# Kernel optimization log

Hardware: AMD Instinct MI355X
Metric: run time of the kernel (lower is better)

Reference implementation:

```python
import jax, jax.numpy as jnp
import numpy as np

N_FACTORS = 4
N_ITERATIONS = 2
N_LAYERS = 2
N_USERS = 50000
N_ITEMS = 50000
EMB_DIM = 128
N_EDGES = 2_000_000
EPS = 1e-12


def setup_inputs() -> dict:
    key = jax.random.key(0)
    k1, k2, k3, k4 = jax.random.split(key, 4)
    n_nodes = N_USERS + N_ITEMS
    return {
        "user_emb": jax.random.normal(k1, (N_USERS, EMB_DIM), dtype=jnp.float32) * 0.1,
        "item_emb": jax.random.normal(k2, (N_ITEMS, EMB_DIM), dtype=jnp.float32) * 0.1,
        "all_h_list": jax.random.randint(k3, (N_EDGES,), 0, n_nodes, dtype=jnp.int32),
        "all_t_list": jax.random.randint(k4, (N_EDGES,), 0, n_nodes, dtype=jnp.int32),
    }


def _l2norm(x):
    # F.normalize(x, dim=1): x / max(||x||_2, eps)
    n = jnp.sqrt(jnp.sum(x * x, axis=1, keepdims=True))
    return x / jnp.maximum(n, EPS)


def _star_routing(user_emb, item_emb, h, t):
    n_nodes = user_emb.shape[0] + item_emb.shape[0]
    E = h.shape[0]
    ego = jnp.concatenate([user_emb, item_emb], axis=0)          # [N, D]
    A_values = jnp.ones((N_FACTORS, E), dtype=ego.dtype)
    all_embeddings = [ego]
    for _layer in range(N_LAYERS):
        ego_chunks = jnp.split(ego, N_FACTORS, axis=1)           # F x [N, D/F]
        layer_chunks = [None] * N_FACTORS
        for it in range(N_ITERATIONS):
            scores = jax.nn.softmax(A_values, axis=0)            # per-edge softmax over factors
            new_vals = []
            for i in range(N_FACTORS):
                v = scores[i]                                    # [E]
                deg = jax.ops.segment_sum(v, h, num_segments=n_nodes)  # row sums of A_i
                d_inv = 1.0 / jnp.sqrt(jnp.maximum(deg, EPS))    # D^{-1/2}
                x = ego_chunks[i] * d_inv[:, None]               # D_col @ e
                # A_i @ x : gather tails, weight by edge value, scatter-add to heads
                x = jax.ops.segment_sum(v[:, None] * x[t], h, num_segments=n_nodes)
                x = x * d_inv[:, None]                           # D_col @ (A @ (D_col @ e))
                layer_chunks[i] = x
                # routing logit update
                head = _l2norm(x[h])                             # [E, D/F]
                tail = _l2norm(ego_chunks[i][t])
                new_vals.append(jnp.sum(head * jnp.tanh(tail), axis=1))
            A_values = A_values + jnp.stack(new_vals, axis=0)
        ego = jnp.concatenate(layer_chunks, axis=1)
        all_embeddings.append(ego)
    # mean over [ego_0, ego_1, ..., ego_L]
    out = jnp.mean(jnp.stack(all_embeddings, axis=1), axis=1)    # [N, D]
    return out


def reference(user_emb, item_emb, all_h_list, all_t_list):
    all_emb = _star_routing(user_emb, item_emb, all_h_list, all_t_list)
    u_g = all_emb[:N_USERS]
    i_g = all_emb[N_USERS:]
    # with pick=False the '_t' (test) path is identical to the train path
    return u_g, i_g, u_g, i_g
```

## Files before the change

kernel.cpp:

```cpp
#include <hip/hip_runtime.h>
#include <cmath>

#define GS_LOOP(i, n) for (int i = blockIdx.x * blockDim.x + threadIdx.x; i < (n); i += gridDim.x * blockDim.x)

constexpr int NUSERS = 50000;
constexpr int NNODES = 100000;
constexpr int EMBD   = 128;
constexpr int NEDGE  = 2000000;
constexpr int NSCAN  = (NNODES + 1023) / 1024;

typedef float          v4f   __attribute__((ext_vector_type(4)));
typedef unsigned short v4u16 __attribute__((ext_vector_type(4)));

__device__ __forceinline__ float bf2f(unsigned short u) {
  union { unsigned int i; float f; } v; v.i = ((unsigned int)u) << 16; return v.f;
}
__device__ __forceinline__ unsigned short f2bf(float x) {
  union { float f; unsigned int i; } v; v.f = x;
  unsigned int r = v.i + 0x7FFFu + ((v.i >> 16) & 1u);
  return (unsigned short)(r >> 16);
}

__global__ __launch_bounds__(256) void init_k(const float4* __restrict__ ue4,
                                              const float4* __restrict__ ie4,
                                              float4* __restrict__ ego0,
                                              ushort4* __restrict__ Pb0,
                                              ushort4* __restrict__ Tnb0) {
  const int j = threadIdx.x & 31;
  const int u = blockIdx.x * 8 + (threadIdx.x >> 5);
  if (u >= NNODES) return;
  const float4 y = (u < NUSERS) ? ue4[(size_t)u * 32 + j]
                                : ie4[(size_t)(u - NUSERS) * 32 + j];
  ego0[(size_t)u * 32 + j] = y;
  Pb0[(size_t)u * 32 + j] = make_ushort4(f2bf(y.x), f2bf(y.y), f2bf(y.z), f2bf(y.w));
  float ss = y.x * y.x + y.y * y.y + y.z * y.z + y.w * y.w;
  ss += __shfl_xor(ss, 1, 64);
  ss += __shfl_xor(ss, 2, 64);
  ss += __shfl_xor(ss, 4, 64);
  const float inv = 1.f / fmaxf(sqrtf(ss), 1e-12f);
  Tnb0[(size_t)u * 32 + j] = make_ushort4(f2bf(tanhf(y.x * inv)), f2bf(tanhf(y.y * inv)),
                                          f2bf(tanhf(y.z * inv)), f2bf(tanhf(y.w * inv)));
}

__global__ void hist_k(const int* __restrict__ h, int* __restrict__ counts) {
  GS_LOOP(e, NEDGE) atomicAdd(&counts[h[e]], 1);
}

__global__ __launch_bounds__(1024) void scan1_k(const int* __restrict__ counts,
                                                int* __restrict__ part,
                                                int* __restrict__ bsum) {
  __shared__ int wsum[16];
  const int tid = threadIdx.x, lane = tid & 63, wid = tid >> 6;
  const int i = blockIdx.x * 1024 + tid;
  int v = (i < NNODES) ? counts[i] : 0;
  #pragma unroll
  for (int off = 1; off < 64; off <<= 1) {
    int y = __shfl_up(v, off, 64);
    if (lane >= off) v += y;
  }
  if (lane == 63) wsum[wid] = v;
  __syncthreads();
  if (wid == 0) {
    int w = (lane < 16) ? wsum[lane] : 0;
    #pragma unroll
    for (int off = 1; off < 16; off <<= 1) {
      int y = __shfl_up(w, off, 64);
      if (lane >= off) w += y;
    }
    if (lane < 16) wsum[lane] = w;
  }
  __syncthreads();
  const int incl = v + (wid ? wsum[wid - 1] : 0);
  if (i < NNODES) part[i] = incl;
  if (tid == 1023) bsum[blockIdx.x] = incl;
}

__global__ __launch_bounds__(128) void scan2_k(const int* __restrict__ bsum,
                                               int* __restrict__ boff) {
  __shared__ int s0[128], s1[128];
  const int tid = threadIdx.x;
  s0[tid] = (tid < NSCAN) ? bsum[tid] : 0;
  __syncthreads();
  int* a = s0; int* b = s1;
  for (int off = 1; off < 128; off <<= 1) {
    const int val = a[tid] + ((tid >= off) ? a[tid - off] : 0);
    b[tid] = val;
    __syncthreads();
    int* tmp = a; a = b; b = tmp;
  }
  boff[tid] = (tid == 0) ? 0 : a[tid - 1];
}

__global__ __launch_bounds__(1024) void scan3_k(const int* __restrict__ part,
                                                const int* __restrict__ boff,
                                                const int* __restrict__ counts,
                                                int* __restrict__ row_ptr,
                                                float* __restrict__ dv0) {
  const int i = blockIdx.x * 1024 + threadIdx.x;
  if (i < NNODES) {
    row_ptr[i + 1] = part[i] + boff[blockIdx.x];
    const float d = rsqrtf(fmaxf(0.25f * (float)counts[i], 1e-12f));
    v4f w = {d, d, d, d};
    *((v4f*)dv0 + i) = w;
  }
  if (i == 0) row_ptr[0] = 0;
}

__global__ void fill_k(const int* __restrict__ h, const int* __restrict__ t,
                       const int* __restrict__ row_ptr, int* __restrict__ cur,
                       int* __restrict__ csr_t) {
  GS_LOOP(e, NEDGE) {
    int u = h[e];
    int pos = row_ptr[u] + atomicAdd(&cur[u], 1);
    csr_t[pos] = t[e];
  }
}

template <int MODE, bool FIRST>
__global__ __launch_bounds__(256) void prop_k(
    const ushort4* __restrict__ Pb4, float4* __restrict__ Q4,
    const float* __restrict__ dv_in, float* __restrict__ dv_out,
    const int* __restrict__ row_ptr, const int* __restrict__ csr_t,
    const float* __restrict__ c, float* __restrict__ A,
    const ushort4* __restrict__ Tnb4, const float4* __restrict__ e0_4,
    const float4* __restrict__ e1_4, float4* __restrict__ o1_4,
    ushort4* __restrict__ Pb1w, ushort4* __restrict__ Tnb1w) {
  const int u = blockIdx.x * 4 + (threadIdx.x >> 6);
  const int l = threadIdx.x & 63;
  const int half = l >> 5;
  const int j = l & 31;
  const int f = j >> 3;
  const int beg = row_ptr[u], end = row_ptr[u + 1];

  float4 acc = make_float4(0.f, 0.f, 0.f, 0.f);
  int p = beg + half;
  for (; p + 14 < end; p += 16) {
    const int t0 = csr_t[p],      t1 = csr_t[p + 2];
    const int t2 = csr_t[p + 4],  t3 = csr_t[p + 6];
    const int t4 = csr_t[p + 8],  t5 = csr_t[p + 10];
    const int t6 = csr_t[p + 12], t7 = csr_t[p + 14];
    const ushort4 y0 = Pb4[(size_t)t0 * 32 + j];
    const ushort4 y1 = Pb4[(size_t)t1 * 32 + j];
    const ushort4 y2 = Pb4[(size_t)t2 * 32 + j];
    const ushort4 y3 = Pb4[(size_t)t3 * 32 + j];
    const ushort4 y4 = Pb4[(size_t)t4 * 32 + j];
    const ushort4 y5 = Pb4[(size_t)t5 * 32 + j];
    const ushort4 y6 = Pb4[(size_t)t6 * 32 + j];
    const ushort4 y7 = Pb4[(size_t)t7 * 32 + j];
    const float c0 = (FIRST ? 0.25f : __builtin_nontemporal_load(c + (size_t)p * 4 + f))        * dv_in[t0 * 4 + f];
    const float c1 = (FIRST ? 0.25f : __builtin_nontemporal_load(c + (size_t)(p + 2) * 4 + f))  * dv_in[t1 * 4 + f];
    const float c2 = (FIRST ? 0.25f : __builtin_nontemporal_load(c + (size_t)(p + 4) * 4 + f))  * dv_in[t2 * 4 + f];
    const float c3 = (FIRST ? 0.25f : __builtin_nontemporal_load(c + (size_t)(p + 6) * 4 + f))  * dv_in[t3 * 4 + f];
    const float c4_ = (FIRST ? 0.25f : __builtin_nontemporal_load(c + (size_t)(p + 8) * 4 + f)) * dv_in[t4 * 4 + f];
    const float c5 = (FIRST ? 0.25f : __builtin_nontemporal_load(c + (size_t)(p + 10) * 4 + f)) * dv_in[t5 * 4 + f];
    const float c6 = (FIRST ? 0.25f : __builtin_nontemporal_load(c + (size_t)(p + 12) * 4 + f)) * dv_in[t6 * 4 + f];
    const float c7 = (FIRST ? 0.25f : __builtin_nontemporal_load(c + (size_t)(p + 14) * 4 + f)) * dv_in[t7 * 4 + f];
    acc.x += c0 * bf2f(y0.x) + c1 * bf2f(y1.x) + c2 * bf2f(y2.x) + c3 * bf2f(y3.x)
           + c4_ * bf2f(y4.x) + c5 * bf2f(y5.x) + c6 * bf2f(y6.x) + c7 * bf2f(y7.x);
    acc.y += c0 * bf2f(y0.y) + c1 * bf2f(y1.y) + c2 * bf2f(y2.y) + c3 * bf2f(y3.y)
           + c4_ * bf2f(y4.y) + c5 * bf2f(y5.y) + c6 * bf2f(y6.y) + c7 * bf2f(y7.y);
    acc.z += c0 * bf2f(y0.z) + c1 * bf2f(y1.z) + c2 * bf2f(y2.z) + c3 * bf2f(y3.z)
           + c4_ * bf2f(y4.z) + c5 * bf2f(y5.z) + c6 * bf2f(y6.z) + c7 * bf2f(y7.z);
    acc.w += c0 * bf2f(y0.w) + c1 * bf2f(y1.w) + c2 * bf2f(y2.w) + c3 * bf2f(y3.w)
           + c4_ * bf2f(y4.w) + c5 * bf2f(y5.w) + c6 * bf2f(y6.w) + c7 * bf2f(y7.w);
  }
  for (; p < end; p += 2) {
    const int tn = csr_t[p];
    const float cf = (FIRST ? 0.25f : __builtin_nontemporal_load(c + (size_t)p * 4 + f)) * dv_in[tn * 4 + f];
    const ushort4 y = Pb4[(size_t)tn * 32 + j];
    acc.x += cf * bf2f(y.x); acc.y += cf * bf2f(y.y);
    acc.z += cf * bf2f(y.z); acc.w += cf * bf2f(y.w);
  }
  acc.x += __shfl_xor(acc.x, 32, 64);
  acc.y += __shfl_xor(acc.y, 32, 64);
  acc.z += __shfl_xor(acc.z, 32, 64);
  acc.w += __shfl_xor(acc.w, 32, 64);
  const float du = dv_in[u * 4 + f];
  const float4 x = make_float4(acc.x * du, acc.y * du, acc.z * du, acc.w * du);

  if (MODE == 2) {
    if (half == 0) {
      const v4f a = __builtin_nontemporal_load((const v4f*)e0_4 + (size_t)u * 32 + j);
      const v4f b = __builtin_nontemporal_load((const v4f*)e1_4 + (size_t)u * 32 + j);
      v4f r = {(a.x + b.x + x.x) * (1.f / 3.f), (a.y + b.y + x.y) * (1.f / 3.f),
               (a.z + b.z + x.z) * (1.f / 3.f), (a.w + b.w + x.w) * (1.f / 3.f)};
      __builtin_nontemporal_store(r, (v4f*)o1_4 + (size_t)u * 32 + j);
    }
    return;
  }
  if (MODE == 1 && half == 0) {
    v4f xq = {x.x, x.y, x.z, x.w};
    __builtin_nontemporal_store(xq, (v4f*)Q4 + (size_t)u * 32 + j);
    v4u16 pb = {f2bf(x.x), f2bf(x.y), f2bf(x.z), f2bf(x.w)};
    __builtin_nontemporal_store(pb, (v4u16*)Pb1w + (size_t)u * 32 + j);
  }

  float ss = x.x * x.x + x.y * x.y + x.z * x.z + x.w * x.w;
  ss += __shfl_xor(ss, 1, 64);
  ss += __shfl_xor(ss, 2, 64);
  ss += __shfl_xor(ss, 4, 64);
  const float inv = 1.f / fmaxf(sqrtf(ss), 1e-12f);
  const float4 xn = make_float4(x.x * inv, x.y * inv, x.z * inv, x.w * inv);
  if (MODE == 1 && half == 0) {
    v4u16 tb = {f2bf(tanhf(xn.x)), f2bf(tanhf(xn.y)), f2bf(tanhf(xn.z)), f2bf(tanhf(xn.w))};
    __builtin_nontemporal_store(tb, (v4u16*)Tnb1w + (size_t)u * 32 + j);
  }

  float dacc = 0.f;
  auto epi = [&](int ei, float s) {
    const float aold = FIRST ? 1.f : __builtin_nontemporal_load(A + (size_t)ei * 4 + f);
    const float anew = aold + s;
    float mx = fmaxf(anew, __shfl_xor(anew, 8, 64));
    mx = fmaxf(mx, __shfl_xor(mx, 16, 64));
    const float ex = __expf(anew - mx);
    float sm = ex + __shfl_xor(ex, 8, 64);
    sm += __shfl_xor(sm, 16, 64);
    const float cv = ex / sm;
    if ((j & 7) == 0) {
      __builtin_nontemporal_store(anew, A + (size_t)ei * 4 + f);
      __builtin_nontemporal_store(cv, (float*)c + (size_t)ei * 4 + f);
      dacc += cv;
    }
  };
  int q = beg + half;
  for (; q + 6 < end; q += 8) {
    const int t0 = csr_t[q],     t1 = csr_t[q + 2];
    const int t2 = csr_t[q + 4], t3 = csr_t[q + 6];
    const ushort4 b0 = Tnb4[(size_t)t0 * 32 + j];
    const ushort4 b1 = Tnb4[(size_t)t1 * 32 + j];
    const ushort4 b2 = Tnb4[(size_t)t2 * 32 + j];
    const ushort4 b3 = Tnb4[(size_t)t3 * 32 + j];
    float s0 = xn.x * bf2f(b0.x) + xn.y * bf2f(b0.y) + xn.z * bf2f(b0.z) + xn.w * bf2f(b0.w);
    float s1 = xn.x * bf2f(b1.x) + xn.y * bf2f(b1.y) + xn.z * bf2f(b1.z) + xn.w * bf2f(b1.w);
    float s2 = xn.x * bf2f(b2.x) + xn.y * bf2f(b2.y) + xn.z * bf2f(b2.z) + xn.w * bf2f(b2.w);
    float s3 = xn.x * bf2f(b3.x) + xn.y * bf2f(b3.y) + xn.z * bf2f(b3.z) + xn.w * bf2f(b3.w);
    #pragma unroll
    for (int m = 1; m < 8; m <<= 1) {
      s0 += __shfl_xor(s0, m, 64); s1 += __shfl_xor(s1, m, 64);
      s2 += __shfl_xor(s2, m, 64); s3 += __shfl_xor(s3, m, 64);
    }
    epi(q, s0); epi(q + 2, s1); epi(q + 4, s2); epi(q + 6, s3);
  }
  for (; q < end; q += 2) {
    const int tn = csr_t[q];
    const ushort4 tb = Tnb4[(size_t)tn * 32 + j];
    float s = xn.x * bf2f(tb.x) + xn.y * bf2f(tb.y) + xn.z * bf2f(tb.z) + xn.w * bf2f(tb.w);
    s += __shfl_xor(s, 1, 64);
    s += __shfl_xor(s, 2, 64);
    s += __shfl_xor(s, 4, 64);
    epi(q, s);
  }
  dacc += __shfl_xor(dacc, 32, 64);
  if (half == 0 && (j & 7) == 0)
    dv_out[u * 4 + f] = rsqrtf(fmaxf(dacc, 1e-12f));
}

extern "C" void kernel_launch(void* const* d_in, const int* in_sizes, int n_in,
                              void* d_out, int out_size, void* d_ws, size_t ws_size,
                              hipStream_t stream) {
  const float* ue = (const float*)d_in[0];
  const float* ie = (const float*)d_in[1];
  const int* h = (const int*)d_in[2];
  const int* t = (const int*)d_in[3];
  float* out = (float*)d_out;
  char* ws = (char*)d_ws;

  size_t off = 0;
  auto alloc = [&](size_t bytes) -> void* {
    void* p = ws + off;
    off += (bytes + 255) & ~size_t(255);
    return p;
  };
  float* ego0  = (float*)alloc(sizeof(float) * (size_t)NNODES * EMBD);
  float* ego1  = (float*)alloc(sizeof(float) * (size_t)NNODES * EMBD);
  float* A     = (float*)alloc(sizeof(float) * 4 * (size_t)NEDGE);
  float* c     = (float*)alloc(sizeof(float) * 4 * (size_t)NEDGE);
  float* dvA   = (float*)alloc(sizeof(float) * NNODES * 4);
  float* dvB   = (float*)alloc(sizeof(float) * NNODES * 4);
  int* row_ptr = (int*)alloc(sizeof(int) * (NNODES + 1));
  int* cur     = (int*)alloc(sizeof(int) * NNODES);
  int* part    = (int*)alloc(sizeof(int) * NNODES);
  int* bsum    = (int*)alloc(sizeof(int) * 128);
  int* boff    = (int*)alloc(sizeof(int) * 128);
  int* csr_t   = (int*)alloc(sizeof(int) * NEDGE);

  float* o1 = out;
  float* o2 = out + (size_t)NNODES * EMBD;
  ushort4* Pb0  = (ushort4*)o1;
  ushort4* Tnb0 = (ushort4*)((char*)o1 + sizeof(unsigned short) * (size_t)NNODES * EMBD);
  ushort4* Pb1  = (ushort4*)o2;
  ushort4* Tnb1 = (ushort4*)((char*)o2 + sizeof(unsigned short) * (size_t)NNODES * EMBD);

  init_k<<<(NNODES + 7) / 8, 256, 0, stream>>>((const float4*)ue, (const float4*)ie,
                                               (float4*)ego0, Pb0, Tnb0);
  hipMemsetAsync(cur, 0, sizeof(int) * NNODES, stream);
  hist_k<<<2048, 256, 0, stream>>>(h, cur);
  scan1_k<<<NSCAN, 1024, 0, stream>>>(cur, part, bsum);
  scan2_k<<<1, 128, 0, stream>>>(bsum, boff);
  scan3_k<<<NSCAN, 1024, 0, stream>>>(part, boff, cur, row_ptr, dvA);
  hipMemsetAsync(cur, 0, sizeof(int) * NNODES, stream);
  fill_k<<<2048, 256, 0, stream>>>(h, t, row_ptr, cur, csr_t);

  prop_k<0, true><<<NNODES / 4, 256, 0, stream>>>(
      Pb0, (float4*)ego1, dvA, dvB, row_ptr, csr_t, c, A, Tnb0,
      (const float4*)ego0, (const float4*)ego1, (float4*)o1, Pb1, Tnb1);
  prop_k<1, false><<<NNODES / 4, 256, 0, stream>>>(
      Pb0, (float4*)ego1, dvB, dvA, row_ptr, csr_t, c, A, Tnb0,
      (const float4*)ego0, (const float4*)ego1, (float4*)o1, Pb1, Tnb1);
  prop_k<0, false><<<NNODES / 4, 256, 0, stream>>>(
      Pb1, (float4*)ego1, dvA, dvB, row_ptr, csr_t, c, A, Tnb1,
      (const float4*)ego0, (const float4*)ego1, (float4*)o1, Pb1, Tnb1);
  prop_k<2, false><<<NNODES / 4, 256, 0, stream>>>(
      Pb1, (float4*)ego1, dvB, dvA, row_ptr, csr_t, c, A, Tnb1,
      (const float4*)ego0, (const float4*)ego1, (float4*)o1, Pb1, Tnb1);

  hipMemcpyAsync(o2, o1, sizeof(float) * (size_t)NNODES * EMBD,
                 hipMemcpyDeviceToDevice, stream);
}
```

Measured before the change: 1.327 ms.

## Split softmax and degree computation into separate kernel and sort CSR tails

Moves the per-edge softmax over factors and the degree reduction out of the propagation kernel's epilogue into a standalone deg_sm_k kernel that reads A as float4 per edge. The propagation kernel now only accumulates routing logits into A, which removes cross-lane shuffles and exp work from the gather loop. It also adds an insertion sort of each CSR row's tail indices, for deterministic order and better gather locality. The cost is three extra launches and extra passes over A and c, plus a serial per-row sort on the device.

```diff
diff --git a/kernel.cpp b/kernel.cpp
--- a/kernel.cpp
+++ b/kernel.cpp
@@ -116,15 +116,63 @@
   }
 }
 
+__global__ void sort_k(const int* __restrict__ row_ptr, int* __restrict__ csr_t) {
+  GS_LOOP(u, NNODES) {
+    const int beg = row_ptr[u], end = row_ptr[u + 1];
+    for (int i = beg + 1; i < end; ++i) {
+      const int v = csr_t[i];
+      int k = i - 1;
+      while (k >= beg && csr_t[k] > v) { csr_t[k + 1] = csr_t[k]; --k; }
+      csr_t[k + 1] = v;
+    }
+  }
+}
+
+__global__ __launch_bounds__(256) void deg_sm_k(const float* __restrict__ A,
+                                                const int* __restrict__ row_ptr,
+                                                float* __restrict__ c,
+                                                float* __restrict__ dv) {
+  const float4* A4 = (const float4*)A;
+  float4* c4 = (float4*)c;
+  const int g = threadIdx.x >> 4;
+  const int lane16 = threadIdx.x & 15;
+  const int u = blockIdx.x * 16 + g;
+  if (u >= NNODES) return;
+  const int beg = row_ptr[u], end = row_ptr[u + 1];
+  float4 acc = make_float4(0.f, 0.f, 0.f, 0.f);
+  for (int p = beg + lane16; p < end; p += 16) {
+    float4 a = A4[p];
+    float m = fmaxf(fmaxf(a.x, a.y), fmaxf(a.z, a.w));
+    float e0 = __expf(a.x - m), e1 = __expf(a.y - m);
+    float e2 = __expf(a.z - m), e3 = __expf(a.w - m);
+    float inv = 1.f / (e0 + e1 + e2 + e3);
+    float4 s = make_float4(e0 * inv, e1 * inv, e2 * inv, e3 * inv);
+    c4[p] = s;
+    acc.x += s.x; acc.y += s.y; acc.z += s.z; acc.w += s.w;
+  }
+  #pragma unroll
+  for (int m = 1; m < 16; m <<= 1) {
+    acc.x += __shfl_xor(acc.x, m, 64);
+    acc.y += __shfl_xor(acc.y, m, 64);
+    acc.z += __shfl_xor(acc.z, m, 64);
+    acc.w += __shfl_xor(acc.w, m, 64);
+  }
+  if (lane16 == 0)
+    ((float4*)dv)[u] = make_float4(rsqrtf(fmaxf(acc.x, 1e-12f)),
+                                   rsqrtf(fmaxf(acc.y, 1e-12f)),
+                                   rsqrtf(fmaxf(acc.z, 1e-12f)),
+                                   rsqrtf(fmaxf(acc.w, 1e-12f)));
+}
+
 template <int MODE, bool FIRST>
 __global__ __launch_bounds__(256) void prop_k(
     const ushort4* __restrict__ Pb4, float4* __restrict__ Q4,
-    const float* __restrict__ dv_in, float* __restrict__ dv_out,
-    const int* __restrict__ row_ptr, const int* __restrict__ csr_t,
-    const float* __restrict__ c, float* __restrict__ A,
-    const ushort4* __restrict__ Tnb4, const float4* __restrict__ e0_4,
-    const float4* __restrict__ e1_4, float4* __restrict__ o1_4,
-    ushort4* __restrict__ Pb1w, ushort4* __restrict__ Tnb1w) {
+    const float* __restrict__ dv_in, const int* __restrict__ row_ptr,
+    const int* __restrict__ csr_t, const float* __restrict__ c,
+    float* __restrict__ A, const ushort4* __restrict__ Tnb4,
+    const float4* __restrict__ e0_4, const float4* __restrict__ e1_4,
+    float4* __restrict__ o1_4, ushort4* __restrict__ Pb1w,
+    ushort4* __restrict__ Tnb1w) {
   const int u = blockIdx.x * 4 + (threadIdx.x >> 6);
   const int l = threadIdx.x & 63;
   const int half = l >> 5;
@@ -206,22 +254,6 @@
     __builtin_nontemporal_store(tb, (v4u16*)Tnb1w + (size_t)u * 32 + j);
   }
 
-  float dacc = 0.f;
-  auto epi = [&](int ei, float s) {
-    const float aold = FIRST ? 1.f : __builtin_nontemporal_load(A + (size_t)ei * 4 + f);
-    const float anew = aold + s;
-    float mx = fmaxf(anew, __shfl_xor(anew, 8, 64));
-    mx = fmaxf(mx, __shfl_xor(mx, 16, 64));
-    const float ex = __expf(anew - mx);
-    float sm = ex + __shfl_xor(ex, 8, 64);
-    sm += __shfl_xor(sm, 16, 64);
-    const float cv = ex / sm;
-    if ((j & 7) == 0) {
-      __builtin_nontemporal_store(anew, A + (size_t)ei * 4 + f);
-      __builtin_nontemporal_store(cv, (float*)c + (size_t)ei * 4 + f);
-      dacc += cv;
-    }
-  };
   int q = beg + half;
   for (; q + 6 < end; q += 8) {
     const int t0 = csr_t[q],     t1 = csr_t[q + 2];
@@ -239,7 +271,19 @@
       s0 += __shfl_xor(s0, m, 64); s1 += __shfl_xor(s1, m, 64);
       s2 += __shfl_xor(s2, m, 64); s3 += __shfl_xor(s3, m, 64);
     }
-    epi(q, s0); epi(q + 2, s1); epi(q + 4, s2); epi(q + 6, s3);
+    if ((j & 7) == 0) {
+      if (FIRST) {
+        A[(size_t)q * 4 + f] = 1.f + s0;
+        A[(size_t)(q + 2) * 4 + f] = 1.f + s1;
+        A[(size_t)(q + 4) * 4 + f] = 1.f + s2;
+        A[(size_t)(q + 6) * 4 + f] = 1.f + s3;
+      } else {
+        A[(size_t)q * 4 + f] += s0;
+        A[(size_t)(q + 2) * 4 + f] += s1;
+        A[(size_t)(q + 4) * 4 + f] += s2;
+        A[(size_t)(q + 6) * 4 + f] += s3;
+      }
+    }
   }
   for (; q < end; q += 2) {
     const int tn = csr_t[q];
@@ -248,11 +292,11 @@
     s += __shfl_xor(s, 1, 64);
     s += __shfl_xor(s, 2, 64);
     s += __shfl_xor(s, 4, 64);
-    epi(q, s);
-  }
-  dacc += __shfl_xor(dacc, 32, 64);
-  if (half == 0 && (j & 7) == 0)
-    dv_out[u * 4 + f] = rsqrtf(fmaxf(dacc, 1e-12f));
+    if ((j & 7) == 0) {
+      if (FIRST) A[(size_t)q * 4 + f] = 1.f + s;
+      else       A[(size_t)q * 4 + f] += s;
+    }
+  }
 }
 
 extern "C" void kernel_launch(void* const* d_in, const int* in_sizes, int n_in,
@@ -300,18 +344,25 @@
   scan3_k<<<NSCAN, 1024, 0, stream>>>(part, boff, cur, row_ptr, dvA);
   hipMemsetAsync(cur, 0, sizeof(int) * NNODES, stream);
   fill_k<<<2048, 256, 0, stream>>>(h, t, row_ptr, cur, csr_t);
+  sort_k<<<512, 256, 0, stream>>>(row_ptr, csr_t);
 
   prop_k<0, true><<<NNODES / 4, 256, 0, stream>>>(
-      Pb0, (float4*)ego1, dvA, dvB, row_ptr, csr_t, c, A, Tnb0,
+      Pb0, (float4*)ego1, dvA, row_ptr, csr_t, c, A, Tnb0,
       (const float4*)ego0, (const float4*)ego1, (float4*)o1, Pb1, Tnb1);
+
+  deg_sm_k<<<(NNODES + 15) / 16, 256, 0, stream>>>(A, row_ptr, c, dvB);
   prop_k<1, false><<<NNODES / 4, 256, 0, stream>>>(
-      Pb0, (float4*)ego1, dvB, dvA, row_ptr, csr_t, c, A, Tnb0,
+      Pb0, (float4*)ego1, dvB, row_ptr, csr_t, c, A, Tnb0,
       (const float4*)ego0, (const float4*)ego1, (float4*)o1, Pb1, Tnb1);
+
+  deg_sm_k<<<(NNODES + 15) / 16, 256, 0, stream>>>(A, row_ptr, c, dvA);
   prop_k<0, false><<<NNODES / 4, 256, 0, stream>>>(
-      Pb1, (float4*)ego1, dvA, dvB, row_ptr, csr_t, c, A, Tnb1,
+      Pb1, (float4*)ego1, dvA, row_ptr, csr_t, c, A, Tnb1,
       (const float4*)ego0, (const float4*)ego1, (float4*)o1, Pb1, Tnb1);
+
+  deg_sm_k<<<(NNODES + 15) / 16, 256, 0, stream>>>(A, row_ptr, c, dvB);
   prop_k<2, false><<<NNODES / 4, 256, 0, stream>>>(
-      Pb1, (float4*)ego1, dvB, dvA, row_ptr, csr_t, c, A, Tnb1,
+      Pb1, (float4*)ego1, dvB, row_ptr, csr_t, c, A, Tnb1,
       (const float4*)ego0, (const float4*)ego1, (float4*)o1, Pb1, Tnb1);
 
   hipMemcpyAsync(o2, o1, sizeof(float) * (size_t)NNODES * EMBD,
```

Result: no change. 1.348 ms (+1.6%).
